# Performance work log

Measured on AMD Instinct MI355X. Metric: run time of the kernel, lower is better.

## Reference

```python
import jax, jax.numpy as jnp
import numpy as np

RATIO_THRESHOLD = 0.8  # Lowe ratio
DISTANCE_THRESHOLD = None
DO_MUTUAL_CHECK = True


def setup_inputs() -> dict:
    key = jax.random.key(0)
    k0, k1 = jax.random.split(key)
    b, d, n, m = 8, 256, 4096, 4096
    d0 = jax.random.normal(k0, (b, d, n), dtype=jnp.float32)
    d1 = jax.random.normal(k1, (b, d, m), dtype=jnp.float32)
    # L2-normalize along descriptor dim so sim is cosine similarity in [-1, 1]
    d0 = d0 / jnp.linalg.norm(d0, axis=1, keepdims=True)
    d1 = d1 / jnp.linalg.norm(d1, axis=1, keepdims=True)
    return {"descriptors0": d0, "descriptors1": d1}


def find_nn(sim, ratio_thresh, distance_thresh):
    k = 2 if ratio_thresh else 1
    sim_nn, ind_nn = jax.lax.top_k(sim, k)  # [b, n, k]
    dist_nn = 2.0 * (1.0 - sim_nn)
    mask = jnp.ones(ind_nn.shape[:-1], dtype=bool)
    if ratio_thresh:
        mask = mask & (dist_nn[..., 0] <= (ratio_thresh ** 2) * dist_nn[..., 1])
    if distance_thresh:
        mask = mask & (dist_nn[..., 0] <= distance_thresh ** 2)
    matches = jnp.where(mask, ind_nn[..., 0], -1)
    scores = jnp.where(mask, (sim_nn[..., 0] + 1.0) / 2.0, 0.0)
    return matches, scores


def mutual_check(m0, m1):
    inds0 = jnp.arange(m0.shape[-1])
    safe = jnp.where(m0 > -1, m0, 0)
    loop = jnp.take_along_axis(m1, safe, axis=-1)
    ok = (m0 > -1) & (inds0 == loop)
    return jnp.where(ok, m0, -1)


def reference(descriptors0, descriptors1):
    # sim[b, n, m] = <desc0[:, :, n], desc1[:, :, m]>
    sim = jnp.einsum("bdn,bdm->bnm", descriptors0, descriptors1)
    matches0, scores0 = find_nn(sim, RATIO_THRESHOLD, DISTANCE_THRESHOLD)
    if DO_MUTUAL_CHECK:
        matches1, _ = find_nn(jnp.swapaxes(sim, 1, 2), RATIO_THRESHOLD, DISTANCE_THRESHOLD)
        matches0 = mutual_check(matches0, matches1)
    return matches0, scores0
```

## Files before the change

kernel.cpp:

```cpp
#include <hip/hip_runtime.h>


typedef unsigned int uint;
typedef unsigned char uchar;
typedef int i32x4 __attribute__((ext_vector_type(4)));
typedef int i32x8 __attribute__((ext_vector_type(8)));
typedef float f32x4 __attribute__((ext_vector_type(4)));

constexpr int B_ = 8, D_ = 256, N_ = 4096;
constexpr int BMR = 128;
constexpr int BNT = 128;
constexpr int CSPLIT = 2;
constexpr int MT_ITERS = (N_ / CSPLIT) / BNT;
constexpr int NSTAGES = MT_ITERS * 2;

constexpr size_t SZ_PANEL = (size_t)B_ * N_ * D_;
constexpr size_t OFF_AT = 0;
constexpr size_t OFF_BT = SZ_PANEL;
constexpr size_t OFF_PR = 2 * SZ_PANEL;
constexpr size_t SZ_PR  = (size_t)4 * B_ * N_ * 8;
constexpr size_t OFF_PC = OFF_PR + SZ_PR;
constexpr size_t SZ_PC  = (size_t)64 * B_ * N_ * 8;
constexpr size_t OFF_M0 = OFF_PC + SZ_PC;
constexpr size_t OFF_S0 = OFF_M0 + (size_t)B_ * N_ * 4;
constexpr size_t OFF_M1 = OFF_S0 + (size_t)B_ * N_ * 4;

__device__ __forceinline__ uchar f2e4m3(float f) {
  uint u = __float_as_uint(f);
  uint s = (u >> 24) & 0x80u;
  uint mag = u & 0x7FFFFFFFu;
  if (mag >= 0x43E00000u) return (uchar)(s | 0x7Eu);
  int e = (int)(mag >> 23) - 127;
  if (e >= -6) {
    uint m = (mag >> 20) & 7u;
    uint rem = mag & 0xFFFFFu;
    m += (rem > 0x80000u) || (rem == 0x80000u && (m & 1u));
    uint ef = (uint)(e + 7);
    if (m == 8u) { m = 0u; ef += 1u; }
    if (ef >= 16u) return (uchar)(s | 0x7Eu);
    return (uchar)(s | (ef << 3) | m);
  } else {
    int q = __float2int_rn(__uint_as_float(mag) * 512.0f);
    if (q >= 8) return (uchar)(s | 0x08u);
    return (uchar)(s | (uint)q);
  }
}

__device__ __forceinline__ void glds16(const void* g, void* l) {
  __builtin_amdgcn_global_load_lds(
      (const __attribute__((address_space(1))) void*)(uintptr_t)(g),
      (__attribute__((address_space(3))) void*)(uint32_t)(uintptr_t)(l),
      16, 0, 0);
}

__device__ __forceinline__ float packkey(float v, uint mask, uint tag) {
  return __uint_as_float((__float_as_uint(v) & mask) | tag);
}

__device__ __forceinline__ float med3f(float a, float b, float c) {
#if __has_builtin(__builtin_amdgcn_fmed3f)
  return __builtin_amdgcn_fmed3f(a, b, c);
#else
  return fmaxf(fminf(a, b), fminf(fmaxf(a, b), c));
#endif
}

__device__ __forceinline__ void top2p(float& s1, float& s2, float k0, float k1) {
  const float mid = med3f(s1, k0, k1);
  s1 = fmaxf(fmaxf(s1, k0), k1);
  s2 = fmaxf(s2, mid);
}

__device__ __forceinline__ void top2merge(float& s1, float& s2, float o1, float o2) {
  const float lo = fminf(s1, o1);
  s1 = fmaxf(s1, o1);
  s2 = fmaxf(lo, fmaxf(s2, o2));
}

__global__ __launch_bounds__(256)
void prep_kernel(const float* __restrict__ in0, const float* __restrict__ in1,
                 uchar* __restrict__ At, uchar* __restrict__ Bt)
{
  __shared__ uchar tile[32][36];
  const int z = blockIdx.z;
  const float* src = (z < 8) ? in0 : in1;
  uchar* dst = (z < 8) ? At : Bt;
  const int b = z & 7;
  const int k0 = blockIdx.y * 32, n0 = blockIdx.x * 32;
  const int t = threadIdx.x;
  const int kl = t >> 3, n4 = (t & 7) * 4;
  const float4 v = *(const float4*)(src + ((size_t)b * D_ + k0 + kl) * N_ + n0 + n4);
  tile[kl][n4 + 0] = f2e4m3(v.x); tile[kl][n4 + 1] = f2e4m3(v.y);
  tile[kl][n4 + 2] = f2e4m3(v.z); tile[kl][n4 + 3] = f2e4m3(v.w);
  __syncthreads();
  const int nl = t >> 3, k4 = (t & 7) * 4;
  uchar4 o;
  o.x = tile[k4 + 0][nl]; o.y = tile[k4 + 1][nl];
  o.z = tile[k4 + 2][nl]; o.w = tile[k4 + 3][nl];
  *(uchar4*)(dst + ((size_t)b * N_ + n0 + nl) * D_ + k0 + k4) = o;
}

__global__ __launch_bounds__(256, 2)
void nn_pass(const uchar* __restrict__ A, const uchar* __restrict__ Bp,
             uint2* __restrict__ partR, uint2* __restrict__ partC)
{
  __shared__ uchar As[BMR * 256];
  __shared__ uchar Bs[2][BNT * 128];

  const int t = threadIdx.x;
  const int bid = blockIdx.x;
  const int b = bid & 7;
  const int rb = (bid >> 3) & 31;
  const int cs = bid >> 8;
  const size_t bOff = (size_t)b * N_ * D_;
  const int r0 = rb * BMR;
  const int c0 = cs * (N_ / CSPLIT);

  const int l = t & 63, wid = t >> 6, wm = wid >> 1, wn = wid & 1;
  const int l15 = l & 15, g = l >> 4;

  const int offA = (t >> 4) * D_ + ((((t & 15) ^ (t >> 4)) & 15) << 4);
  const int offB = (t >> 3) * D_ + ((((t & 7) ^ ((t >> 3) & 7))) << 4);
  const int lds0 = t * 16;

  const uchar* Ab = A  + bOff + (size_t)r0 * D_;
  const uchar* Bb = Bp + bOff + (size_t)c0 * D_;

  #pragma unroll
  for (int i = 0; i < 8; ++i)
    glds16(Ab + offA + i * 4096, (char*)As + lds0 + i * 4096);
  #pragma unroll
  for (int i = 0; i < 4; ++i)
    glds16(Bb + offB + i * 8192, (char*)Bs[0] + lds0 + i * 4096);
  __syncthreads();

  const float NEG = __uint_as_float(0xFF800000u);
  float rs1[4][4], rs2[4][4];
  #pragma unroll
  for (int mi = 0; mi < 4; ++mi)
    #pragma unroll
    for (int rg = 0; rg < 4; ++rg) { rs1[mi][rg] = NEG; rs2[mi][rg] = NEG; }

  float cp1[4], cp2[4];

  #pragma unroll 1
  for (int mt = 0; mt < MT_ITERS; ++mt) {
    if (mt > 0 && g == 0) {
      const int cbp = (mt - 1) * BNT + wn * 64;
      #pragma unroll
      for (int ni = 0; ni < 4; ++ni)
        partC[((size_t)(rb * 2 + wm) * B_ + b) * N_ + c0 + cbp + ni * 16 + l15] =
            make_uint2(__float_as_uint(cp1[ni]), __float_as_uint(cp2[ni]));
    }

    f32x4 acc[4][4];
    #pragma unroll
    for (int mi = 0; mi < 4; ++mi)
      #pragma unroll
      for (int ni = 0; ni < 4; ++ni) acc[mi][ni] = (f32x4){0.f, 0.f, 0.f, 0.f};

    #pragma unroll
    for (int ks = 0; ks < 2; ++ks) {
      const int s = mt * 2 + ks;
      if (s + 1 < NSTAGES) {
        const int src = ((s + 1) >> 1) * BNT * D_ + ((s + 1) & 1) * 128;
        #pragma unroll
        for (int i = 0; i < 4; ++i)
          glds16(Bb + src + offB + i * 8192, (char*)Bs[(s + 1) & 1] + lds0 + i * 4096);
      }

      i32x8 af[4], bf[4];
      #pragma unroll
      for (int mi = 0; mi < 4; ++mi) {
        const uchar* base = As + (wm * 64 + mi * 16 + l15) * 256;
        const int gx = ks * 8 + 2 * g;
        const i32x4 p0 = *(const i32x4*)(base + (((gx    ) ^ l15) << 4));
        const i32x4 p1 = *(const i32x4*)(base + (((gx + 1) ^ l15) << 4));
        af[mi] = __builtin_shufflevector(p0, p1, 0, 1, 2, 3, 4, 5, 6, 7);
      }
      #pragma unroll
      for (int ni = 0; ni < 4; ++ni) {
        const uchar* base = (const uchar*)Bs[s & 1] + (wn * 64 + ni * 16 + l15) * 128;
        const int gx = 2 * g;
        const i32x4 p0 = *(const i32x4*)(base + (((gx    ) ^ (l15 & 7)) << 4));
        const i32x4 p1 = *(const i32x4*)(base + (((gx + 1) ^ (l15 & 7)) << 4));
        bf[ni] = __builtin_shufflevector(p0, p1, 0, 1, 2, 3, 4, 5, 6, 7);
      }

      __builtin_amdgcn_s_setprio(1);
      #pragma unroll
      for (int mi = 0; mi < 4; ++mi)
        #pragma unroll
        for (int ni = 0; ni < 4; ++ni)
          acc[mi][ni] = __builtin_amdgcn_mfma_scale_f32_16x16x128_f8f6f4(
              af[mi], bf[ni], acc[mi][ni], 0, 0, 0, 127, 0, 127);
      __builtin_amdgcn_s_setprio(0);

      if (ks == 1) {
        const int colb = mt * BNT + wn * 64;
        const uint tg0 = (uint)(2047 - (colb + l15));
        #pragma unroll
        for (int mi = 0; mi < 4; ++mi)
          #pragma unroll
          for (int rg = 0; rg < 4; ++rg) {
            const float k0 = packkey(acc[mi][0][rg], 0xFFFFF800u, tg0);
            const float k1 = packkey(acc[mi][1][rg], 0xFFFFF800u, tg0 - 16);
            const float k2 = packkey(acc[mi][2][rg], 0xFFFFF800u, tg0 - 32);
            const float k3 = packkey(acc[mi][3][rg], 0xFFFFF800u, tg0 - 48);
            top2p(rs1[mi][rg], rs2[mi][rg], k0, k1);
            top2p(rs1[mi][rg], rs2[mi][rg], k2, k3);
          }
        const uint tgb = (uint)(63 - g * 4);
        #pragma unroll
        for (int ni = 0; ni < 4; ++ni) {
          float c1 = NEG, c2 = NEG;
          #pragma unroll
          for (int mi = 0; mi < 4; ++mi) {
            const float k0 = packkey(acc[mi][ni][0], 0xFFFFFFC0u, tgb - (uint)(mi * 16));
            const float k1 = packkey(acc[mi][ni][1], 0xFFFFFFC0u, tgb - (uint)(mi * 16 + 1));
            const float k2 = packkey(acc[mi][ni][2], 0xFFFFFFC0u, tgb - (uint)(mi * 16 + 2));
            const float k3 = packkey(acc[mi][ni][3], 0xFFFFFFC0u, tgb - (uint)(mi * 16 + 3));
            top2p(c1, c2, k0, k1);
            top2p(c1, c2, k2, k3);
          }
          #pragma unroll
          for (int off = 16; off <= 32; off <<= 1) {
            const float o1 = __shfl_xor(c1, off);
            const float o2 = __shfl_xor(c2, off);
            top2merge(c1, c2, o1, o2);
          }
          cp1[ni] = c1; cp2[ni] = c2;
        }
      }
      __syncthreads();
    }
  }

  if (g == 0) {
    const int cbp = (MT_ITERS - 1) * BNT + wn * 64;
    #pragma unroll
    for (int ni = 0; ni < 4; ++ni)
      partC[((size_t)(rb * 2 + wm) * B_ + b) * N_ + c0 + cbp + ni * 16 + l15] =
          make_uint2(__float_as_uint(cp1[ni]), __float_as_uint(cp2[ni]));
  }

  #pragma unroll
  for (int off = 1; off < 16; off <<= 1) {
    #pragma unroll
    for (int mi = 0; mi < 4; ++mi)
      #pragma unroll
      for (int rg = 0; rg < 4; ++rg) {
        const float o1 = __shfl_xor(rs1[mi][rg], off);
        const float o2 = __shfl_xor(rs2[mi][rg], off);
        top2merge(rs1[mi][rg], rs2[mi][rg], o1, o2);
      }
  }
  if (l15 == 0) {
    #pragma unroll
    for (int mi = 0; mi < 4; ++mi)
      #pragma unroll
      for (int rg = 0; rg < 4; ++rg)
        partR[((size_t)(cs * 2 + wn) * B_ + b) * N_ + r0 + wm * 64 + mi * 16 + g * 4 + rg] =
            make_uint2(__float_as_uint(rs1[mi][rg]), __float_as_uint(rs2[mi][rg]));
  }
}

__global__ __launch_bounds__(256)
void merge_kernel(const uint2* __restrict__ pR, const uint2* __restrict__ pC,
                  int* __restrict__ m0, float* __restrict__ s0, int* __restrict__ m1)
{
  const int tid = blockIdx.x * 256 + threadIdx.x;
  if (tid >= 2 * B_ * N_) return;
  const int dir = tid >> 15;
  const int i = tid & (B_ * N_ - 1);
  const float NEG = __uint_as_float(0xFF800000u);

  if (dir == 0) {
    float s1 = NEG, s2 = NEG; int bs = 0;
    #pragma unroll
    for (int sl = 0; sl < 4; ++sl) {
      const uint2 v = pR[(size_t)sl * B_ * N_ + i];
      const float o1 = __uint_as_float(v.x), o2 = __uint_as_float(v.y);
      bs = (o1 > s1) ? sl : bs;
      top2merge(s1, s2, o1, o2);
    }
    const uint k1 = __float_as_uint(s1);
    const int col = (bs >> 1) * 2048 + 2047 - (int)(k1 & 0x7FFu);
    const float v1 = __uint_as_float(k1 & 0xFFFFF800u);
    const float v2 = __uint_as_float(__float_as_uint(s2) & 0xFFFFF800u);
    const bool ok = (1.0f - v1) <= 0.64f * (1.0f - v2);
    m0[i] = ok ? col : -1;
    s0[i] = ok ? (v1 + 1.0f) * 0.5f : 0.0f;
  } else {
    float s1 = NEG, s2 = NEG; int bs = 0;
    #pragma unroll 8
    for (int sl = 0; sl < 64; ++sl) {
      const uint2 v = pC[(size_t)sl * B_ * N_ + i];
      const float o1 = __uint_as_float(v.x), o2 = __uint_as_float(v.y);
      bs = (o1 > s1) ? sl : bs;
      top2merge(s1, s2, o1, o2);
    }
    const uint k1 = __float_as_uint(s1);
    const int row = bs * 64 + 63 - (int)(k1 & 0x3Fu);
    const float v1 = __uint_as_float(k1 & 0xFFFFFFC0u);
    const float v2 = __uint_as_float(__float_as_uint(s2) & 0xFFFFFFC0u);
    const bool ok = (1.0f - v1) <= 0.64f * (1.0f - v2);
    m1[i] = ok ? row : -1;
  }
}

__global__ __launch_bounds__(256)
void finalize_kernel(const int* __restrict__ m0, const float* __restrict__ s0,
                     const int* __restrict__ m1, float* __restrict__ out)
{
  const int idx = blockIdx.x * 256 + threadIdx.x;
  if (idx >= B_ * N_) return;
  const int b = idx >> 12;
  const int n = idx & (N_ - 1);
  const int mm = m0[idx];
  int res = -1;
  if (mm > -1 && m1[((size_t)b << 12) + mm] == n) res = mm;
  out[idx] = (float)res;
  out[B_ * N_ + idx] = s0[idx];
}

extern "C" void kernel_launch(void* const* d_in, const int* in_sizes, int n_in,
                              void* d_out, int out_size, void* d_ws, size_t ws_size,
                              hipStream_t stream)
{
  const float* d0 = (const float*)d_in[0];
  const float* d1 = (const float*)d_in[1];
  float* out = (float*)d_out;

  uchar* At = (uchar*)((char*)d_ws + OFF_AT);
  uchar* Bt = (uchar*)((char*)d_ws + OFF_BT);
  uint2* PR = (uint2*)((char*)d_ws + OFF_PR);
  uint2* PC = (uint2*)((char*)d_ws + OFF_PC);
  int*   m0 = (int*)  ((char*)d_ws + OFF_M0);
  float* s0 = (float*)((char*)d_ws + OFF_S0);
  int*   m1 = (int*)  ((char*)d_ws + OFF_M1);

  prep_kernel<<<dim3(N_ / 32, D_ / 32, 16), 256, 0, stream>>>(d0, d1, At, Bt);
  nn_pass<<<dim3(B_ * (N_ / BMR) * CSPLIT), 256, 0, stream>>>(At, Bt, PR, PC);
  merge_kernel<<<dim3(2 * B_ * N_ / 256), 256, 0, stream>>>(PR, PC, m0, s0, m1);
  finalize_kernel<<<dim3(B_ * N_ / 256), 256, 0, stream>>>(m0, s0, m1, out);
}
```

Before: 86.88 us.

## Pre-swizzle FP8 panels into MFMA fragment layout and keep A in registers

The prep kernel now writes the FP8 panels directly in MFMA-fragment order (128-row tiles), so each lane's operand is a contiguous 16-byte chunk. nn_pass drops the A shared-memory panel and loads the A fragments once into registers for the whole column sweep. B tiles are streamed with contiguous global-to-LDS copies and read without XOR swizzling, and the k-step loop is restructured with interleaved B-fragment loads and MFMAs. This is meant to cut LDS footprint and traffic and to simplify address math, at the cost of higher register pressure and a more coupled layout contract between prep and the GEMM.

```diff
diff --git a/kernel.cpp b/kernel.cpp
--- a/kernel.cpp
+++ b/kernel.cpp
@@ -12,7 +12,7 @@
 constexpr int BNT = 128;
 constexpr int CSPLIT = 2;
 constexpr int MT_ITERS = (N_ / CSPLIT) / BNT;
-constexpr int NSTAGES = MT_ITERS * 2;
+
 
 constexpr size_t SZ_PANEL = (size_t)B_ * N_ * D_;
 constexpr size_t OFF_AT = 0;
@@ -81,57 +81,79 @@
 void prep_kernel(const float* __restrict__ in0, const float* __restrict__ in1,
                  uchar* __restrict__ At, uchar* __restrict__ Bt)
 {
-  __shared__ uchar tile[32][36];
-  const int z = blockIdx.z;
-  const float* src = (z < 8) ? in0 : in1;
-  uchar* dst = (z < 8) ? At : Bt;
-  const int b = z & 7;
-  const int k0 = blockIdx.y * 32, n0 = blockIdx.x * 32;
+  __shared__ uchar tile[128][44];
+  const int bz = blockIdx.z;
+  const float* src = (bz < 8) ? in0 : in1;
+  uchar* dst = (bz < 8) ? At : Bt;
+  const int b = bz & 7;
+  const int n0 = blockIdx.x * 128;
+  const int k0b = blockIdx.y * 32;
   const int t = threadIdx.x;
-  const int kl = t >> 3, n4 = (t & 7) * 4;
-  const float4 v = *(const float4*)(src + ((size_t)b * D_ + k0 + kl) * N_ + n0 + n4);
-  tile[kl][n4 + 0] = f2e4m3(v.x); tile[kl][n4 + 1] = f2e4m3(v.y);
-  tile[kl][n4 + 2] = f2e4m3(v.z); tile[kl][n4 + 3] = f2e4m3(v.w);
+
+  const int kq = t >> 5;
+  const int n4 = (t & 31) * 4;
+  const float* pin = src + ((size_t)b * D_ + k0b + kq * 4) * N_ + n0 + n4;
+  float4 v[4];
+  #pragma unroll
+  for (int j = 0; j < 4; ++j) v[j] = *(const float4*)(pin + (size_t)j * N_);
+  #pragma unroll
+  for (int i = 0; i < 4; ++i) {
+    uchar4 o = make_uchar4(f2e4m3(((const float*)&v[0])[i]),
+                           f2e4m3(((const float*)&v[1])[i]),
+                           f2e4m3(((const float*)&v[2])[i]),
+                           f2e4m3(((const float*)&v[3])[i]));
+    *(uchar4*)&tile[n4 + i][kq * 4] = o;
+  }
   __syncthreads();
-  const int nl = t >> 3, k4 = (t & 7) * 4;
-  uchar4 o;
-  o.x = tile[k4 + 0][nl]; o.y = tile[k4 + 1][nl];
-  o.z = tile[k4 + 2][nl]; o.w = tile[k4 + 3][nl];
-  *(uchar4*)(dst + ((size_t)b * N_ + n0 + nl) * D_ + k0 + k4) = o;
+
+  const int nl = t & 127, h = t >> 7;
+  const int kg = k0b + h * 16;
+  const int ks = kg >> 7, g = (kg >> 5) & 3, hh = (kg >> 4) & 1;
+  const int q = (nl >> 6) & 1, r4 = (nl >> 4) & 3, i16 = nl & 15;
+  i32x4 val;
+  #pragma unroll
+  for (int j = 0; j < 4; ++j)
+    val[j] = *(const int*)&tile[nl][h * 16 + j * 4];
+  uchar* po = dst + (size_t)b * (N_ * D_) + (size_t)blockIdx.x * 32768 +
+              ks * 16384 + ((q * 4 + r4) * 2 + hh) * 1024 + (g * 16 + i16) * 16;
+  *(i32x4*)po = val;
 }
 
 __global__ __launch_bounds__(256, 2)
 void nn_pass(const uchar* __restrict__ A, const uchar* __restrict__ Bp,
              uint2* __restrict__ partR, uint2* __restrict__ partC)
 {
-  __shared__ uchar As[BMR * 256];
-  __shared__ uchar Bs[2][BNT * 128];
+  __shared__ uchar Bs[2][16384];
 
   const int t = threadIdx.x;
   const int bid = blockIdx.x;
   const int b = bid & 7;
   const int rb = (bid >> 3) & 31;
   const int cs = bid >> 8;
-  const size_t bOff = (size_t)b * N_ * D_;
+  const size_t bOff = (size_t)b * (N_ * D_);
   const int r0 = rb * BMR;
-  const int c0 = cs * (N_ / CSPLIT);
 
   const int l = t & 63, wid = t >> 6, wm = wid >> 1, wn = wid & 1;
   const int l15 = l & 15, g = l >> 4;
-
-  const int offA = (t >> 4) * D_ + ((((t & 15) ^ (t >> 4)) & 15) << 4);
-  const int offB = (t >> 3) * D_ + ((((t & 7) ^ ((t >> 3) & 7))) << 4);
   const int lds0 = t * 16;
 
-  const uchar* Ab = A  + bOff + (size_t)r0 * D_;
-  const uchar* Bb = Bp + bOff + (size_t)c0 * D_;
-
-  #pragma unroll
-  for (int i = 0; i < 8; ++i)
-    glds16(Ab + offA + i * 4096, (char*)As + lds0 + i * 4096);
+  const uchar* Aseg = A + bOff + (size_t)rb * 32768;
+  const uchar* Bb = Bp + bOff + (size_t)cs * 524288;
+
   #pragma unroll
   for (int i = 0; i < 4; ++i)
-    glds16(Bb + offB + i * 8192, (char*)Bs[0] + lds0 + i * 4096);
+    glds16(Bb + i * 4096 + lds0, (char*)Bs[0] + i * 4096 + lds0);
+
+  i32x8 af[2][4];
+  #pragma unroll
+  for (int ks = 0; ks < 2; ++ks)
+    #pragma unroll
+    for (int mi = 0; mi < 4; ++mi) {
+      const uchar* p = Aseg + ks * 16384 + ((wm * 4 + mi) * 2) * 1024 + l * 16;
+      const i32x4 lo = *(const i32x4*)p;
+      const i32x4 hi = *(const i32x4*)(p + 1024);
+      af[ks][mi] = __builtin_shufflevector(lo, hi, 0, 1, 2, 3, 4, 5, 6, 7);
+    }
   __syncthreads();
 
   const float NEG = __uint_as_float(0xFF800000u);
@@ -142,14 +164,17 @@
     for (int rg = 0; rg < 4; ++rg) { rs1[mi][rg] = NEG; rs2[mi][rg] = NEG; }
 
   float cp1[4], cp2[4];
+  const char* aB = (const char*)Bs[0] + l * 16;
 
   #pragma unroll 1
   for (int mt = 0; mt < MT_ITERS; ++mt) {
+    const uchar* Bct = Bb + (size_t)mt * 32768;
+
     if (mt > 0 && g == 0) {
       const int cbp = (mt - 1) * BNT + wn * 64;
       #pragma unroll
       for (int ni = 0; ni < 4; ++ni)
-        partC[((size_t)(rb * 2 + wm) * B_ + b) * N_ + c0 + cbp + ni * 16 + l15] =
+        partC[((size_t)(rb * 2 + wm) * B_ + b) * N_ + cs * 2048 + cbp + ni * 16 + l15] =
             make_uint2(__float_as_uint(cp1[ni]), __float_as_uint(cp2[ni]));
     }
 
@@ -160,87 +185,85 @@
       for (int ni = 0; ni < 4; ++ni) acc[mi][ni] = (f32x4){0.f, 0.f, 0.f, 0.f};
 
     #pragma unroll
-    for (int ks = 0; ks < 2; ++ks) {
-      const int s = mt * 2 + ks;
-      if (s + 1 < NSTAGES) {
-        const int src = ((s + 1) >> 1) * BNT * D_ + ((s + 1) & 1) * 128;
-        #pragma unroll
-        for (int i = 0; i < 4; ++i)
-          glds16(Bb + src + offB + i * 8192, (char*)Bs[(s + 1) & 1] + lds0 + i * 4096);
+    for (int i = 0; i < 4; ++i)
+      glds16(Bct + 16384 + i * 4096 + lds0, (char*)Bs[1] + i * 4096 + lds0);
+
+    #pragma unroll
+    for (int ni = 0; ni < 4; ++ni) {
+      const int imm = ((wn * 4 + ni) * 2) * 1024;
+      const i32x4 lo = *(const i32x4*)(aB + imm);
+      const i32x4 hi = *(const i32x4*)(aB + imm + 1024);
+      const i32x8 bf = __builtin_shufflevector(lo, hi, 0, 1, 2, 3, 4, 5, 6, 7);
+      __builtin_amdgcn_s_setprio(1);
+      #pragma unroll
+      for (int mi = 0; mi < 4; ++mi)
+        acc[mi][ni] = __builtin_amdgcn_mfma_scale_f32_16x16x128_f8f6f4(
+            af[0][mi], bf, acc[mi][ni], 0, 0, 0, 127, 0, 127);
+      __builtin_amdgcn_s_setprio(0);
+    }
+    __syncthreads();
+
+    if (mt + 1 < MT_ITERS) {
+      #pragma unroll
+      for (int i = 0; i < 4; ++i)
+        glds16(Bct + 32768 + i * 4096 + lds0, (char*)Bs[0] + i * 4096 + lds0);
+    }
+    #pragma unroll
+    for (int ni = 0; ni < 4; ++ni) {
+      const int imm = 16384 + ((wn * 4 + ni) * 2) * 1024;
+      const i32x4 lo = *(const i32x4*)(aB + imm);
+      const i32x4 hi = *(const i32x4*)(aB + imm + 1024);
+      const i32x8 bf = __builtin_shufflevector(lo, hi, 0, 1, 2, 3, 4, 5, 6, 7);
+      __builtin_amdgcn_s_setprio(1);
+      #pragma unroll
+      for (int mi = 0; mi < 4; ++mi)
+        acc[mi][ni] = __builtin_amdgcn_mfma_scale_f32_16x16x128_f8f6f4(
+            af[1][mi], bf, acc[mi][ni], 0, 0, 0, 127, 0, 127);
+      __builtin_amdgcn_s_setprio(0);
+    }
+
+    const int colb = mt * BNT + wn * 64;
+    const uint tg0 = (uint)(2047 - (colb + l15));
+    #pragma unroll
+    for (int mi = 0; mi < 4; ++mi)
+      #pragma unroll
+      for (int rg = 0; rg < 4; ++rg) {
+        const float k0 = packkey(acc[mi][0][rg], 0xFFFFF800u, tg0);
+        const float k1 = packkey(acc[mi][1][rg], 0xFFFFF800u, tg0 - 16);
+        const float k2 = packkey(acc[mi][2][rg], 0xFFFFF800u, tg0 - 32);
+        const float k3 = packkey(acc[mi][3][rg], 0xFFFFF800u, tg0 - 48);
+        top2p(rs1[mi][rg], rs2[mi][rg], k0, k1);
+        top2p(rs1[mi][rg], rs2[mi][rg], k2, k3);
       }
-
-      i32x8 af[4], bf[4];
+    const uint tgb = (uint)(63 - g * 4);
+    #pragma unroll
+    for (int ni = 0; ni < 4; ++ni) {
+      float c1 = NEG, c2 = NEG;
       #pragma unroll
       for (int mi = 0; mi < 4; ++mi) {
-        const uchar* base = As + (wm * 64 + mi * 16 + l15) * 256;
-        const int gx = ks * 8 + 2 * g;
-        const i32x4 p0 = *(const i32x4*)(base + (((gx    ) ^ l15) << 4));
-        const i32x4 p1 = *(const i32x4*)(base + (((gx + 1) ^ l15) << 4));
-        af[mi] = __builtin_shufflevector(p0, p1, 0, 1, 2, 3, 4, 5, 6, 7);
+        const float k0 = packkey(acc[mi][ni][0], 0xFFFFFFC0u, tgb - (uint)(mi * 16));
+        const float k1 = packkey(acc[mi][ni][1], 0xFFFFFFC0u, tgb - (uint)(mi * 16 + 1));
+        const float k2 = packkey(acc[mi][ni][2], 0xFFFFFFC0u, tgb - (uint)(mi * 16 + 2));
+        const float k3 = packkey(acc[mi][ni][3], 0xFFFFFFC0u, tgb - (uint)(mi * 16 + 3));
+        top2p(c1, c2, k0, k1);
+        top2p(c1, c2, k2, k3);
       }
       #pragma unroll
-      for (int ni = 0; ni < 4; ++ni) {
-        const uchar* base = (const uchar*)Bs[s & 1] + (wn * 64 + ni * 16 + l15) * 128;
-        const int gx = 2 * g;
-        const i32x4 p0 = *(const i32x4*)(base + (((gx    ) ^ (l15 & 7)) << 4));
-        const i32x4 p1 = *(const i32x4*)(base + (((gx + 1) ^ (l15 & 7)) << 4));
-        bf[ni] = __builtin_shufflevector(p0, p1, 0, 1, 2, 3, 4, 5, 6, 7);
+      for (int off = 16; off <= 32; off <<= 1) {
+        const float o1 = __shfl_xor(c1, off);
+        const float o2 = __shfl_xor(c2, off);
+        top2merge(c1, c2, o1, o2);
       }
-
-      __builtin_amdgcn_s_setprio(1);
-      #pragma unroll
-      for (int mi = 0; mi < 4; ++mi)
-        #pragma unroll
-        for (int ni = 0; ni < 4; ++ni)
-          acc[mi][ni] = __builtin_amdgcn_mfma_scale_f32_16x16x128_f8f6f4(
-              af[mi], bf[ni], acc[mi][ni], 0, 0, 0, 127, 0, 127);
-      __builtin_amdgcn_s_setprio(0);
-
-      if (ks == 1) {
-        const int colb = mt * BNT + wn * 64;
-        const uint tg0 = (uint)(2047 - (colb + l15));
-        #pragma unroll
-        for (int mi = 0; mi < 4; ++mi)
-          #pragma unroll
-          for (int rg = 0; rg < 4; ++rg) {
-            const float k0 = packkey(acc[mi][0][rg], 0xFFFFF800u, tg0);
-            const float k1 = packkey(acc[mi][1][rg], 0xFFFFF800u, tg0 - 16);
-            const float k2 = packkey(acc[mi][2][rg], 0xFFFFF800u, tg0 - 32);
-            const float k3 = packkey(acc[mi][3][rg], 0xFFFFF800u, tg0 - 48);
-            top2p(rs1[mi][rg], rs2[mi][rg], k0, k1);
-            top2p(rs1[mi][rg], rs2[mi][rg], k2, k3);
-          }
-        const uint tgb = (uint)(63 - g * 4);
-        #pragma unroll
-        for (int ni = 0; ni < 4; ++ni) {
-          float c1 = NEG, c2 = NEG;
-          #pragma unroll
-          for (int mi = 0; mi < 4; ++mi) {
-            const float k0 = packkey(acc[mi][ni][0], 0xFFFFFFC0u, tgb - (uint)(mi * 16));
-            const float k1 = packkey(acc[mi][ni][1], 0xFFFFFFC0u, tgb - (uint)(mi * 16 + 1));
-            const float k2 = packkey(acc[mi][ni][2], 0xFFFFFFC0u, tgb - (uint)(mi * 16 + 2));
-            const float k3 = packkey(acc[mi][ni][3], 0xFFFFFFC0u, tgb - (uint)(mi * 16 + 3));
-            top2p(c1, c2, k0, k1);
-            top2p(c1, c2, k2, k3);
-          }
-          #pragma unroll
-          for (int off = 16; off <= 32; off <<= 1) {
-            const float o1 = __shfl_xor(c1, off);
-            const float o2 = __shfl_xor(c2, off);
-            top2merge(c1, c2, o1, o2);
-          }
-          cp1[ni] = c1; cp2[ni] = c2;
-        }
-      }
-      __syncthreads();
-    }
+      cp1[ni] = c1; cp2[ni] = c2;
+    }
+    __syncthreads();
   }
 
   if (g == 0) {
     const int cbp = (MT_ITERS - 1) * BNT + wn * 64;
     #pragma unroll
     for (int ni = 0; ni < 4; ++ni)
-      partC[((size_t)(rb * 2 + wm) * B_ + b) * N_ + c0 + cbp + ni * 16 + l15] =
+      partC[((size_t)(rb * 2 + wm) * B_ + b) * N_ + cs * 2048 + cbp + ni * 16 + l15] =
           make_uint2(__float_as_uint(cp1[ni]), __float_as_uint(cp2[ni]));
   }
 
@@ -340,7 +363,7 @@
   float* s0 = (float*)((char*)d_ws + OFF_S0);
   int*   m1 = (int*)  ((char*)d_ws + OFF_M1);
 
-  prep_kernel<<<dim3(N_ / 32, D_ / 32, 16), 256, 0, stream>>>(d0, d1, At, Bt);
+  prep_kernel<<<dim3(N_ / 128, D_ / 32, 16), 256, 0, stream>>>(d0, d1, At, Bt);
   nn_pass<<<dim3(B_ * (N_ / BMR) * CSPLIT), 256, 0, stream>>>(At, Bt, PR, PC);
   merge_kernel<<<dim3(2 * B_ * N_ / 256), 256, 0, stream>>>(PR, PC, m0, s0, m1);
   finalize_kernel<<<dim3(B_ * N_ / 256), 256, 0, stream>>>(m0, s0, m1, out);
```

After: 81.70 us. -6.0%, faster.
